# Performance work log

Hardware: AMD Instinct MI355X
Metric: run time of the kernel (lower is better)

Reference implementation:

```python
import jax, jax.numpy as jnp
from jax import lax
import numpy as np

B, H, W = 16, 512, 512
OPENING_R, EROSION_R, DILATION_R = 5, 2, 1
MIN_SIZE, AREA_THRESHOLD = 2000, 300
INF = np.int32(2 ** 30)


def _disk(r):
    # skimage.morphology.disk: x^2 + y^2 <= r^2 on a (2r+1)^2 grid
    y, x = np.mgrid[-r:r + 1, -r:r + 1]
    return jnp.asarray((x * x + y * y <= r * r).astype(np.float32))


D_OPEN, D_ERODE, D_DILATE = _disk(OPENING_R), _disk(EROSION_R), _disk(DILATION_R)


def _conv2(x, k):
    return lax.conv_general_dilated(x[None, None], k[None, None], (1, 1), 'VALID')[0, 0]


def _erode(fg, se):
    # skimage binary_erosion uses border_value=True (image border does not erode)
    r = se.shape[0] // 2
    x = jnp.pad(fg.astype(jnp.float32), r, constant_values=1.0)
    return _conv2(x, se) >= se.sum() - 0.5


def _dilate(fg, se):
    # skimage binary_dilation uses border_value=False
    r = se.shape[0] // 2
    x = jnp.pad(fg.astype(jnp.float32), r, constant_values=0.0)
    return _conv2(x, se) > 0.5


def _seg_cummin(v, reset, axis, reverse):
    # segmented cumulative-min: scan resets wherever `reset` is True (background)
    def comb(a, b):
        av, af = a
        bv, bf = b
        return jnp.where(bf, bv, jnp.minimum(av, bv)), af | bf

    vv, _ = lax.associative_scan(comb, (v, reset), axis=axis, reverse=reverse)
    return vv


def _label(fg):
    # 4-connectivity connected-component labeling via min-label propagation.
    # Each fg pixel starts with its raveled index; alternating row/col segmented
    # cummin sweeps run under while_loop until a fixed point (root id per comp).
    h, w = fg.shape
    idx = jnp.arange(h * w, dtype=jnp.int32).reshape(h, w)
    lab0 = jnp.where(fg, idx, INF)
    bg = ~fg

    def sweep(l):
        for axis in (1, 0):
            for rev in (False, True):
                l = jnp.where(fg, _seg_cummin(l, bg, axis, rev), INF)
        return l

    def body(c):
        l, _ = c
        nl = sweep(l)
        return nl, jnp.array_equal(nl, l)

    lab, _ = lax.while_loop(lambda c: ~c[1], body, (lab0, jnp.array(False)))
    seg = jnp.where(fg, lab, 0).ravel()
    sizes = jax.ops.segment_sum(fg.astype(jnp.int32).ravel(), seg, num_segments=h * w)
    ncomp = jnp.sum(sizes > 0)
    return lab, sizes, ncomp


def _remove_small_objects(fg, min_size, guard):
    lab, sizes, ncomp = _label(fg)
    px = sizes[jnp.where(fg, lab, 0)]  # component size at every fg pixel
    kept = fg & (px >= min_size)
    # original only removes small objects when label(...).max() > 1
    return jnp.where(ncomp > 1, kept, fg) if guard else kept


def _pipeline(mask):
    fg = mask > 0
    fg = _remove_small_objects(fg, MIN_SIZE, True)
    # remove_small_holes == ~remove_small_objects(~fg, area_threshold + 1)
    fg = ~_remove_small_objects(~fg, AREA_THRESHOLD + 1, False)
    fg = _erode(fg, D_ERODE)
    fg = _dilate(_erode(fg, D_OPEN), D_OPEN)  # binary_opening
    fg = _remove_small_objects(fg, MIN_SIZE, True)
    fg = _dilate(fg, D_DILATE)
    return fg.astype(jnp.float32)  # original casts to int; float32 kept for vjp parity


def setup_inputs() -> dict:
    key = jax.random.key(0)
    # blobby binary masks: threshold bilinearly-upsampled low-res noise so that
    # realistic large connected components (> min_size px) exist
    low = jax.random.uniform(key, (B, H // 16, W // 16), dtype=jnp.float32)
    blob = jax.image.resize(low, (B, H, W), method='bilinear')
    return {'inputs': (blob > 0.5).astype(jnp.float32)}


def reference(inputs):
    return jax.vmap(_pipeline)(inputs)
```

## Files before the change

kernel.cpp:

```cpp
#include <hip/hip_runtime.h>
#include <stdint.h>

#define BATCH 16
#define H 512
#define W 512
#define HW (H * W)
#define NTOT (BATCH * HW)
#define NWORDS (NTOT / 64)

#define TPB 256
#define NBLKW ((NWORDS + TPB - 1) / TPB)

#define SROWS 16
#define SWORDS 128
#define SPIX 8192
#define NSTRIPS (NWORDS / SWORDS)

__device__ __forceinline__ int find_root_c(int* L, int x) {
    int r = x, p = L[r];
    while (p != r) { r = p; p = L[r]; }
    if (L[x] != r) atomicMin(&L[x], r);
    return r;
}

__device__ void merge_uf(int* L, int a, int b) {
    while (true) {
        a = find_root_c(L, a);
        b = find_root_c(L, b);
        if (a == b) return;
        int lo = a < b ? a : b;
        int hi = a < b ? b : a;
        int old = atomicMin(&L[hi], lo);
        if (old == hi) return;
        a = lo; b = old;
    }
}

__device__ __forceinline__ int find_root_lds(int* P, int x) {
    int r = x, p = P[r];
    while (p != r) { r = p; p = P[r]; }
    return r;
}

__device__ void merge_lds(int* P, int a, int b) {
    while (true) {
        a = find_root_lds(P, a);
        b = find_root_lds(P, b);
        if (a == b) return;
        int lo = a < b ? a : b;
        int hi = a < b ? b : a;
        int old = atomicMin(&P[hi], lo);
        if (old == hi) return;
        a = lo; b = old;
    }
}

__device__ __forceinline__ int start_of(uint64_t m, int i, int cv, int base) {
    uint64_t below = i ? ((~m) & ((1ull << i) - 1)) : 0ull;
    if (below == 0) return (cv >= 0) ? cv : base;
    int hz = 63 - __builtin_clzll(below);
    return base + hz + 1;
}

__device__ uint64_t keep_word(const uint64_t* __restrict__ bits,
                              const int* __restrict__ carry, const int* __restrict__ L,
                              const int* __restrict__ sizes, const int* __restrict__ ncomp,
                              int minsz, int gw) {
    uint64_t m = bits[gw];
    uint64_t res = m;
    if (m && ncomp[gw >> 12] > 1) {
        int cv = carry[gw];
        int base = gw << 6;
        while (m) {
            int s = __builtin_ctzll(m);
            uint64_t rest = m >> s;
            uint64_t nr = ~rest;
            int len = nr ? __builtin_ctzll(nr) : (64 - s);
            uint64_t piece = ((len >= 64) ? ~0ull : ((1ull << len) - 1)) << s;
            int start = (s == 0 && cv >= 0) ? cv : (base + s);
            if (sizes[L[start]] < minsz) res &= ~piece;
            m &= ~piece;
        }
    }
    return res;
}

__device__ uint64_t fill_word(const uint64_t* __restrict__ bits,
                              const int* __restrict__ carry, const int* __restrict__ L,
                              const int* __restrict__ sizes, int minsz, int gw) {
    uint64_t fg = bits[gw];
    uint64_t bg = ~fg;
    uint64_t res = fg;
    int cv = carry[gw];
    int base = gw << 6;
    while (bg) {
        int s = __builtin_ctzll(bg);
        uint64_t rest = bg >> s;
        uint64_t nr = ~rest;
        int len = nr ? __builtin_ctzll(nr) : (64 - s);
        uint64_t piece = ((len >= 64) ? ~0ull : ((1ull << len) - 1)) << s;
        int start = (s == 0 && cv >= 0) ? cv : (base + s);
        if (sizes[L[start]] < minsz) res |= piece;
        bg &= ~piece;
    }
    return res;
}

template <int R, bool ERODE>
__device__ uint64_t morph_word_lds(const uint64_t* buf, int lrow, int w, int gyTop) {
    const uint64_t BORDER = ERODE ? ~0ull : 0ull;
    uint64_t res = ERODE ? ~0ull : 0ull;
#pragma unroll
    for (int dy = -R; dy <= R; ++dy) {
        int lr = lrow + dy;
        int gy = gyTop + lr;
        if (gy < 0 || gy >= H) continue;
        int v = R * R - dy * dy;
        int kx = 0;
        while ((kx + 1) * (kx + 1) <= v) ++kx;
        uint64_t cur = buf[lr * 8 + w];
        uint64_t prv = (w > 0) ? buf[lr * 8 + w - 1] : BORDER;
        uint64_t nxt = (w < 7) ? buf[lr * 8 + w + 1] : BORDER;
        uint64_t acc = cur;
#pragma unroll
        for (int dx = 1; dx <= kx; ++dx) {
            uint64_t right = (cur >> dx) | (nxt << (64 - dx));
            uint64_t left  = (cur << dx) | (prv >> (64 - dx));
            if (ERODE) acc &= right & left;
            else       acc |= right | left;
        }
        if (ERODE) res &= acc;
        else       res |= acc;
    }
    return res;
}

__device__ void strip_ccl_body(uint64_t m, uint64_t* sw, int* scarry, int* par,
                               int blk, int t,
                               int* __restrict__ carry, int* __restrict__ L,
                               int* __restrict__ sizes, int* __restrict__ ncomp) {
    sw[t] = m;
    __syncthreads();

    if (t < SROWS) {
        int cv = -1;
        for (int i = 0; i < 8; ++i) {
            int lw = t * 8 + i;
            scarry[lw] = cv;
            uint64_t w = sw[lw];
            if (w >> 63) {
                uint64_t z = ~w;
                if (z == 0) { if (cv < 0) cv = lw << 6; }
                else { int hz = 63 - __builtin_clzll(z); cv = (lw << 6) + hz + 1; }
            } else cv = -1;
        }
    }
    __syncthreads();

    int cv = scarry[t];
    carry[blk * SWORDS + t] = (cv >= 0) ? (blk * SPIX + cv) : -1;
    int lbase = t << 6;
    uint64_t starts = m & ~((m << 1) | ((cv >= 0) ? 1ull : 0ull));
    uint64_t ss = starts;
    while (ss) {
        int s = __builtin_ctzll(ss);
        par[lbase + s] = lbase + s;
        ss &= ss - 1;
    }
    __syncthreads();

    if (t >= 8 && m) {
        uint64_t up = sw[t - 8];
        uint64_t cand = m & up;
        if (cand) {
            uint64_t curprev = (t & 7) ? sw[t - 1] : 0ull;
            uint64_t upprev  = (t & 7) ? sw[t - 9] : 0ull;
            uint64_t curl = (m << 1) | (curprev >> 63);
            uint64_t upl  = (up << 1) | (upprev >> 63);
            cand &= ~(curl & upl);
            int cvu = scarry[t - 8];
            while (cand) {
                int i = __builtin_ctzll(cand);
                int sP = start_of(m, i, cv, lbase);
                int sQ = start_of(up, i, cvu, lbase - 512);
                merge_lds(par, sP, sQ);
                cand &= cand - 1;
            }
        }
    }
    __syncthreads();

    int gpix = blk * SPIX;
    ss = starts;
    while (ss) {
        int s = __builtin_ctzll(ss);
        int ls = lbase + s;
        int r = find_root_lds(par, ls);
        L[gpix + ls] = gpix + r;
        if (r == ls) sizes[gpix + ls] = 0;
        ss &= ss - 1;
    }
    if (t == 0 && (blk & 31) == 0) ncomp[blk >> 5] = 0;
}


__global__ void k_thresh_pack4(const float4* __restrict__ in4,
                               uint64_t* __restrict__ bits) {
    int q = blockIdx.x * blockDim.x + threadIdx.x;
    if (q >= NTOT / 4) return;
    float4 v = in4[q];
    uint32_t nib = (v.x > 0.0f ? 1u : 0u) | (v.y > 0.0f ? 2u : 0u) |
                   (v.z > 0.0f ? 4u : 0u) | (v.w > 0.0f ? 8u : 0u);
    uint64_t val = (uint64_t)nib << (4 * (threadIdx.x & 15));
    val |= __shfl_xor(val, 1);
    val |= __shfl_xor(val, 2);
    val |= __shfl_xor(val, 4);
    val |= __shfl_xor(val, 8);
    if ((threadIdx.x & 15) == 0) bits[q >> 4] = val;
}

__global__ void k_strip_ccl(const uint64_t* __restrict__ bits, int inv,
                            int* __restrict__ carry, int* __restrict__ L,
                            int* __restrict__ sizes, int* __restrict__ ncomp) {
    __shared__ uint64_t sw[SWORDS];
    __shared__ int scarry[SWORDS];
    __shared__ int par[SPIX];
    int blk = blockIdx.x;
    int t = threadIdx.x;
    uint64_t inv64 = inv ? ~0ull : 0ull;
    uint64_t m = bits[blk * SWORDS + t] ^ inv64;
    strip_ccl_body(m, sw, scarry, par, blk, t, carry, L, sizes, ncomp);
}

__global__ void k_keep_strip(const uint64_t* __restrict__ bits,
                             const int* __restrict__ carryIn, const int* __restrict__ Lin,
                             const int* __restrict__ sizesIn, const int* __restrict__ ncompIn,
                             uint64_t* __restrict__ outBits,
                             int* __restrict__ carryOut, int* __restrict__ Lout,
                             int* __restrict__ sizesOut, int* __restrict__ ncompOut) {
    __shared__ uint64_t sw[SWORDS];
    __shared__ int scarry[SWORDS];
    __shared__ int par[SPIX];
    int blk = blockIdx.x;
    int t = threadIdx.x;
    int gw = blk * SWORDS + t;
    uint64_t kw = keep_word(bits, carryIn, Lin, sizesIn, ncompIn, 2000, gw);
    outBits[gw] = kw;
    strip_ccl_body(~kw, sw, scarry, par, blk, t, carryOut, Lout, sizesOut, ncompOut);
}

__global__ void k_merge_bound(const uint64_t* __restrict__ bits, int inv,
                              const int* __restrict__ carry, int* __restrict__ L) {
    int tid = threadIdx.x;
    if (tid >= 248) return;
    int img = blockIdx.x;
    int y = ((tid >> 3) + 1) * SROWS;
    int w = tid & 7;
    int gw = img * 4096 + y * 8 + w;
    uint64_t inv64 = inv ? ~0ull : 0ull;
    uint64_t cur = bits[gw] ^ inv64;
    uint64_t up  = bits[gw - 8] ^ inv64;
    uint64_t cand = cur & up;
    if (!cand) return;
    uint64_t curprev = w ? (bits[gw - 1] ^ inv64) : 0ull;
    uint64_t upprev  = w ? (bits[gw - 9] ^ inv64) : 0ull;
    uint64_t curl = (cur << 1) | (curprev >> 63);
    uint64_t upl  = (up << 1)  | (upprev >> 63);
    cand &= ~(curl & upl);
    if (!cand) return;
    int cvc = carry[gw], cvu = carry[gw - 8];
    int base = gw << 6;
    while (cand) {
        int i = __builtin_ctzll(cand);
        int sP = start_of(cur, i, cvc, base);
        int sQ = start_of(up, i, cvu, base - W);
        merge_uf(L, sP, sQ);
        cand &= cand - 1;
    }
}

__global__ void k_flatten_count(const uint64_t* __restrict__ bits, int inv,
                                const int* __restrict__ carry, int* __restrict__ L,
                                int* __restrict__ sizes, int* __restrict__ ncomp) {
    __shared__ int hk[128];
    __shared__ int hv[128];
    for (int i = threadIdx.x; i < 128; i += TPB) { hk[i] = -1; hv[i] = 0; }
    __syncthreads();

    int gw = blockIdx.x * blockDim.x + threadIdx.x;
    if (gw < NWORDS) {
        uint64_t inv64 = inv ? ~0ull : 0ull;
        uint64_t m = bits[gw] ^ inv64;
        if (m) {
            int cv = carry[gw];
            int base = gw << 6;
            while (m) {
                int s = __builtin_ctzll(m);
                uint64_t rest = m >> s;
                uint64_t nr = ~rest;
                int len = nr ? __builtin_ctzll(nr) : (64 - s);
                uint64_t piece = ((len >= 64) ? ~0ull : ((1ull << len) - 1)) << s;
                bool initial = !(s == 0 && cv >= 0);
                int start = initial ? (base + s) : cv;
                int r = find_root_c(L, start);
                if (initial && r == start) atomicAdd(&ncomp[gw >> 12], 1);
                int cnt = __popcll(piece);
                uint32_t h = ((uint32_t)r * 2654435761u) >> 25;
                bool done = false;
                for (int tt = 0; tt < 16; ++tt) {
                    int slot = (h + tt) & 127;
                    int k = hk[slot];
                    if (k == -1) k = atomicCAS(&hk[slot], -1, r);
                    if (k == -1 || k == r) { atomicAdd(&hv[slot], cnt); done = true; break; }
                }
                if (!done) atomicAdd(&sizes[r], cnt);
                m &= ~piece;
            }
        }
    }
    __syncthreads();
    for (int i = threadIdx.x; i < 128; i += TPB)
        if (hk[i] != -1) atomicAdd(&sizes[hk[i]], hv[i]);
}

__global__ void k_fill_morph_ccl(const uint64_t* __restrict__ bits,
                                 const int* __restrict__ carryB, const int* __restrict__ LB,
                                 const int* __restrict__ sizesB,
                                 uint64_t* __restrict__ bits3,
                                 int* __restrict__ carryA, int* __restrict__ LA,
                                 int* __restrict__ sizesA, int* __restrict__ ncompA) {
    __shared__ uint64_t sw[SWORDS];
    __shared__ int scarry[SWORDS];
    __shared__ union {
        int par[SPIX];
        struct { uint64_t A[320]; uint64_t B[320]; } mo;
    } U;
    int s = blockIdx.x;
    int t = threadIdx.x;
    int img = s >> 5, si = s & 31;
    int gyTop = si * 16 - 12;

    for (int lw = t; lw < 320; lw += SWORDS) {
        int gy = gyTop + (lw >> 3);
        int w = lw & 7;
        uint64_t v = 0;
        if (gy >= 0 && gy < H)
            v = fill_word(bits, carryB, LB, sizesB, 301, img * 4096 + gy * 8 + w);
        U.mo.A[lw] = v;
    }
    __syncthreads();
    for (int lw = t; lw < 320; lw += SWORDS) {
        int lr = lw >> 3;
        if (lr >= 2 && lr <= 37) U.mo.B[lw] = morph_word_lds<2, true>(U.mo.A, lr, lw & 7, gyTop);
    }
    __syncthreads();
    for (int lw = t; lw < 320; lw += SWORDS) {
        int lr = lw >> 3;
        if (lr >= 7 && lr <= 32) U.mo.A[lw] = morph_word_lds<5, true>(U.mo.B, lr, lw & 7, gyTop);
    }
    __syncthreads();
    for (int lw = t; lw < 320; lw += SWORDS) {
        int lr = lw >> 3;
        if (lr >= 12 && lr <= 27) U.mo.B[lw] = morph_word_lds<5, false>(U.mo.A, lr, lw & 7, gyTop);
    }
    __syncthreads();
    uint64_t m3 = U.mo.B[t + 96];
    bits3[s * SWORDS + t] = m3;
    strip_ccl_body(m3, sw, scarry, U.par, s, t, carryA, LA, sizesA, ncompA);
}

__global__ void k_keep_dilate_float(const uint64_t* __restrict__ bits,
                                    const int* __restrict__ carry, const int* __restrict__ L,
                                    const int* __restrict__ sizes, const int* __restrict__ ncomp,
                                    float* __restrict__ out) {
    __shared__ uint64_t kb[10 * 8];
    __shared__ uint64_t db[8 * 8];
    int blk = blockIdx.x;
    int img = blk >> 6;
    int s = blk & 63;
    int y0 = s * 8;
    int t = threadIdx.x;

    if (t < 80) {
        int lr = t >> 3;
        int w = t & 7;
        int gy = y0 - 1 + lr;
        uint64_t v = 0;
        if (gy >= 0 && gy < H)
            v = keep_word(bits, carry, L, sizes, ncomp, 2000, img * 4096 + gy * 8 + w);
        kb[t] = v;
    }
    __syncthreads();
    if (t < 64) {
        int r = t >> 3, w = t & 7;
        uint64_t cur = kb[(r + 1) * 8 + w];
        uint64_t up  = kb[r * 8 + w];
        uint64_t dn  = kb[(r + 2) * 8 + w];
        uint64_t prv = w ? kb[(r + 1) * 8 + w - 1] : 0ull;
        uint64_t nxt = (w < 7) ? kb[(r + 1) * 8 + w + 1] : 0ull;
        db[t] = cur | up | dn | (cur << 1) | (prv >> 63) | (cur >> 1) | (nxt << 63);
    }
    __syncthreads();

    int q0 = t * 16;
    uint64_t wd = db[q0 >> 6];
    int sh = q0 & 63;
    float4* o = (float4*)(out + (size_t)img * HW + (size_t)y0 * W + q0);
#pragma unroll
    for (int k = 0; k < 4; ++k) {
        uint32_t nib = (uint32_t)(wd >> (sh + k * 4)) & 0xFu;
        float4 f;
        f.x = (nib & 1u) ? 1.0f : 0.0f;
        f.y = (nib & 2u) ? 1.0f : 0.0f;
        f.z = (nib & 4u) ? 1.0f : 0.0f;
        f.w = (nib & 8u) ? 1.0f : 0.0f;
        o[k] = f;
    }
}

extern "C" void kernel_launch(void* const* d_in, const int* in_sizes, int n_in,
                              void* d_out, int out_size, void* d_ws, size_t ws_size,
                              hipStream_t stream) {
    const float* in = (const float*)d_in[0];
    float* out = (float*)d_out;

    uint8_t* ws = (uint8_t*)d_ws;
    int* LA      = (int*)ws;
    int* sizesA  = (int*)(ws + (size_t)NTOT * 4);
    int* LB      = (int*)(ws + (size_t)NTOT * 8);
    int* sizesB  = (int*)(ws + (size_t)NTOT * 12);
    uint64_t* bits1 = (uint64_t*)(ws + (size_t)NTOT * 16);
    uint64_t* bits2 = bits1 + NWORDS;
    uint64_t* bits3 = bits2 + NWORDS;
    int* carryA = (int*)(bits3 + NWORDS);
    int* carryB = carryA + NWORDS;
    int* ncompA = carryB + NWORDS;
    int* ncompB = ncompA + BATCH;

    k_thresh_pack4<<<(NTOT / 4 + TPB - 1) / TPB, TPB, 0, stream>>>((const float4*)in, bits1);

    k_strip_ccl<<<NSTRIPS, SWORDS, 0, stream>>>(bits1, 0, carryA, LA, sizesA, ncompA);
    k_merge_bound<<<BATCH, 256, 0, stream>>>(bits1, 0, carryA, LA);
    k_flatten_count<<<NBLKW, TPB, 0, stream>>>(bits1, 0, carryA, LA, sizesA, ncompA);

    k_keep_strip<<<NSTRIPS, SWORDS, 0, stream>>>(bits1, carryA, LA, sizesA, ncompA,
                                                 bits2, carryB, LB, sizesB, ncompB);
    k_merge_bound<<<BATCH, 256, 0, stream>>>(bits2, 1, carryB, LB);
    k_flatten_count<<<NBLKW, TPB, 0, stream>>>(bits2, 1, carryB, LB, sizesB, ncompB);

    k_fill_morph_ccl<<<NSTRIPS, SWORDS, 0, stream>>>(bits2, carryB, LB, sizesB,
                                                     bits3, carryA, LA, sizesA, ncompA);
    k_merge_bound<<<BATCH, 256, 0, stream>>>(bits3, 0, carryA, LA);
    k_flatten_count<<<NBLKW, TPB, 0, stream>>>(bits3, 0, carryA, LA, sizesA, ncompA);

    k_keep_dilate_float<<<BATCH * 64, TPB, 0, stream>>>(bits3, carryA, LA, sizesA, ncompA, out);
}
```

Baseline: 201.3 us.

## Fuse whole pipeline into one persistent per-image kernel with run-based labels

Replaces the chain of about eleven kernel launches with a single kernel using one 1024-thread workgroup per image, running every stage back to back separated by workgroup barriers. Union-find labels are now indexed by run id rather than pixel, built with a prefix-scan over run counts, and merged with workgroup-scope atomics in global memory. The morphology stages read whole images from global memory instead of haloed LDS strips. This removes launch overhead and inter-kernel round trips, but uses only 16 workgroups on a many-CU GPU, so most of the device sits idle and the serial work per image grows.

```diff
diff --git a/kernel.cpp b/kernel.cpp
--- a/kernel.cpp
+++ b/kernel.cpp
@@ -7,120 +7,109 @@
 #define HW (H * W)
 #define NTOT (BATCH * HW)
 #define NWORDS (NTOT / 64)
-
-#define TPB 256
-#define NBLKW ((NWORDS + TPB - 1) / TPB)
-
+#define IMGW 4096
+#define IMGQ 65536
 #define SROWS 16
 #define SWORDS 128
-#define SPIX 8192
-#define NSTRIPS (NWORDS / SWORDS)
-
-__device__ __forceinline__ int find_root_c(int* L, int x) {
-    int r = x, p = L[r];
-    while (p != r) { r = p; p = L[r]; }
-    if (L[x] != r) atomicMin(&L[x], r);
+#define MAXR 4096
+#define NR (BATCH * 32 * MAXR)
+#define WALK_LIMIT (1 << 16)
+
+static __device__ __forceinline__ int aldw(const int* p) {
+    return __hip_atomic_load((int*)p, __ATOMIC_RELAXED, __HIP_MEMORY_SCOPE_WORKGROUP);
+}
+static __device__ __forceinline__ int aminw(int* p, int v) {
+    return __hip_atomic_fetch_min(p, v, __ATOMIC_RELAXED, __HIP_MEMORY_SCOPE_WORKGROUP);
+}
+static __device__ __forceinline__ int aaddw(int* p, int v) {
+    return __hip_atomic_fetch_add(p, v, __ATOMIC_RELAXED, __HIP_MEMORY_SCOPE_WORKGROUP);
+}
+
+static __device__ __forceinline__ int find_root(int* L, int x) {
+    int r = x, p = aldw(&L[r]), g = 0;
+    while (p != r && ++g < WALK_LIMIT) { r = p; p = aldw(&L[r]); }
+    if (aldw(&L[x]) != r) aminw(&L[x], r);
     return r;
 }
 
-__device__ void merge_uf(int* L, int a, int b) {
-    while (true) {
-        a = find_root_c(L, a);
-        b = find_root_c(L, b);
+static __device__ void merge_uf(int* L, int a, int b) {
+    int g = 0;
+    while (++g < WALK_LIMIT) {
+        a = find_root(L, a);
+        b = find_root(L, b);
         if (a == b) return;
         int lo = a < b ? a : b;
         int hi = a < b ? b : a;
-        int old = atomicMin(&L[hi], lo);
+        int old = aminw(&L[hi], lo);
         if (old == hi) return;
         a = lo; b = old;
     }
 }
 
-__device__ __forceinline__ int find_root_lds(int* P, int x) {
-    int r = x, p = P[r];
-    while (p != r) { r = p; p = P[r]; }
-    return r;
-}
-
-__device__ void merge_lds(int* P, int a, int b) {
-    while (true) {
-        a = find_root_lds(P, a);
-        b = find_root_lds(P, b);
-        if (a == b) return;
-        int lo = a < b ? a : b;
-        int hi = a < b ? b : a;
-        int old = atomicMin(&P[hi], lo);
-        if (old == hi) return;
-        a = lo; b = old;
-    }
-}
-
-__device__ __forceinline__ int start_of(uint64_t m, int i, int cv, int base) {
+static __device__ __forceinline__ int run_of(uint64_t m, int i, int cvrid, int wr) {
     uint64_t below = i ? ((~m) & ((1ull << i) - 1)) : 0ull;
-    if (below == 0) return (cv >= 0) ? cv : base;
-    int hz = 63 - __builtin_clzll(below);
-    return base + hz + 1;
-}
-
-__device__ uint64_t keep_word(const uint64_t* __restrict__ bits,
-                              const int* __restrict__ carry, const int* __restrict__ L,
-                              const int* __restrict__ sizes, const int* __restrict__ ncomp,
-                              int minsz, int gw) {
-    uint64_t m = bits[gw];
-    uint64_t res = m;
-    if (m && ncomp[gw >> 12] > 1) {
-        int cv = carry[gw];
-        int base = gw << 6;
-        while (m) {
-            int s = __builtin_ctzll(m);
-            uint64_t rest = m >> s;
-            uint64_t nr = ~rest;
-            int len = nr ? __builtin_ctzll(nr) : (64 - s);
-            uint64_t piece = ((len >= 64) ? ~0ull : ((1ull << len) - 1)) << s;
-            int start = (s == 0 && cv >= 0) ? cv : (base + s);
-            if (sizes[L[start]] < minsz) res &= ~piece;
-            m &= ~piece;
-        }
-    }
-    return res;
-}
-
-__device__ uint64_t fill_word(const uint64_t* __restrict__ bits,
-                              const int* __restrict__ carry, const int* __restrict__ L,
-                              const int* __restrict__ sizes, int minsz, int gw) {
-    uint64_t fg = bits[gw];
-    uint64_t bg = ~fg;
-    uint64_t res = fg;
-    int cv = carry[gw];
-    int base = gw << 6;
-    while (bg) {
-        int s = __builtin_ctzll(bg);
-        uint64_t rest = bg >> s;
+    if (below == 0) return (cvrid >= 0) ? cvrid : wr;
+    int s = 64 - __builtin_clzll(below);
+    uint64_t starts = m & ~((m << 1) | ((cvrid >= 0) ? 1ull : 0ull));
+    return wr + __popcll(starts & ((1ull << s) - 1));
+}
+
+static __device__ __forceinline__ int run_of_l(uint64_t m, int i, int cv,
+                                               uint64_t starts, int wb) {
+    uint64_t below = i ? ((~m) & ((1ull << i) - 1)) : 0ull;
+    if (below == 0) return (cv >= 0) ? cv : wb;
+    int s = 64 - __builtin_clzll(below);
+    return wb + __popcll(starts & ((1ull << s) - 1));
+}
+
+static __device__ uint64_t keep_word_g(uint64_t m, int cvg, int wrg,
+                                       const int* L, const int* S, int minsz) {
+    uint64_t res = m, rem = m; int rk = 0;
+    while (rem) {
+        int s = __builtin_ctzll(rem);
+        uint64_t rest = rem >> s;
         uint64_t nr = ~rest;
         int len = nr ? __builtin_ctzll(nr) : (64 - s);
         uint64_t piece = ((len >= 64) ? ~0ull : ((1ull << len) - 1)) << s;
-        int start = (s == 0 && cv >= 0) ? cv : (base + s);
-        if (sizes[L[start]] < minsz) res |= piece;
-        bg &= ~piece;
+        bool ini = !(s == 0 && cvg >= 0);
+        int rid = ini ? (wrg + rk) : cvg; rk += ini ? 1 : 0;
+        if (aldw(&S[aldw(&L[rid])]) < minsz) res &= ~piece;
+        rem &= ~piece;
     }
     return res;
 }
 
+static __device__ uint64_t fill_word_g(uint64_t fg, int cvg, int wrg,
+                                       const int* L, const int* S, int minsz) {
+    uint64_t res = fg, rem = ~fg; int rk = 0;
+    while (rem) {
+        int s = __builtin_ctzll(rem);
+        uint64_t rest = rem >> s;
+        uint64_t nr = ~rest;
+        int len = nr ? __builtin_ctzll(nr) : (64 - s);
+        uint64_t piece = ((len >= 64) ? ~0ull : ((1ull << len) - 1)) << s;
+        bool ini = !(s == 0 && cvg >= 0);
+        int rid = ini ? (wrg + rk) : cvg; rk += ini ? 1 : 0;
+        if (aldw(&S[aldw(&L[rid])]) < minsz) res |= piece;
+        rem &= ~piece;
+    }
+    return res;
+}
+
 template <int R, bool ERODE>
-__device__ uint64_t morph_word_lds(const uint64_t* buf, int lrow, int w, int gyTop) {
+static __device__ uint64_t morph_word_g(const uint64_t* ib, int row, int w) {
     const uint64_t BORDER = ERODE ? ~0ull : 0ull;
     uint64_t res = ERODE ? ~0ull : 0ull;
 #pragma unroll
     for (int dy = -R; dy <= R; ++dy) {
-        int lr = lrow + dy;
-        int gy = gyTop + lr;
+        int gy = row + dy;
         if (gy < 0 || gy >= H) continue;
         int v = R * R - dy * dy;
         int kx = 0;
         while ((kx + 1) * (kx + 1) <= v) ++kx;
-        uint64_t cur = buf[lr * 8 + w];
-        uint64_t prv = (w > 0) ? buf[lr * 8 + w - 1] : BORDER;
-        uint64_t nxt = (w < 7) ? buf[lr * 8 + w + 1] : BORDER;
+        uint64_t cur = ib[gy * 8 + w];
+        uint64_t prv = (w > 0) ? ib[gy * 8 + w - 1] : BORDER;
+        uint64_t nxt = (w < 7) ? ib[gy * 8 + w + 1] : BORDER;
         uint64_t acc = cur;
 #pragma unroll
         for (int dx = 1; dx <= kx; ++dx) {
@@ -135,286 +124,268 @@
     return res;
 }
 
-__device__ void strip_ccl_body(uint64_t m, uint64_t* sw, int* scarry, int* par,
-                               int blk, int t,
-                               int* __restrict__ carry, int* __restrict__ L,
-                               int* __restrict__ sizes, int* __restrict__ ncomp) {
-    sw[t] = m;
-    __syncthreads();
-
-    if (t < SROWS) {
-        int cv = -1;
-        for (int i = 0; i < 8; ++i) {
-            int lw = t * 8 + i;
-            scarry[lw] = cv;
-            uint64_t w = sw[lw];
-            if (w >> 63) {
-                uint64_t z = ~w;
-                if (z == 0) { if (cv < 0) cv = lw << 6; }
-                else { int hz = 63 - __builtin_clzll(z); cv = (lw << 6) + hz + 1; }
-            } else cv = -1;
-        }
-    }
-    __syncthreads();
-
-    int cv = scarry[t];
-    carry[blk * SWORDS + t] = (cv >= 0) ? (blk * SPIX + cv) : -1;
-    int lbase = t << 6;
-    uint64_t starts = m & ~((m << 1) | ((cv >= 0) ? 1ull : 0ull));
-    uint64_t ss = starts;
-    while (ss) {
-        int s = __builtin_ctzll(ss);
-        par[lbase + s] = lbase + s;
-        ss &= ss - 1;
-    }
-    __syncthreads();
-
-    if (t >= 8 && m) {
-        uint64_t up = sw[t - 8];
-        uint64_t cand = m & up;
+static __device__ void ccl_image(int img, int t, const uint64_t* bits, uint64_t inv64,
+                                 int* carry, int* wordrun, int* L, int* S, int* ncomp,
+                                 uint64_t (*ssw)[SWORDS], int (*sscar)[SWORDS],
+                                 int (*scnt)[SWORDS], int (*swb)[SWORDS], int* wsum) {
+    int sg = t >> 7, tt = t & 127;
+    int lane = t & 63;
+    if (t == 0) ncomp[img] = 0;
+
+    for (int sr = 0; sr < 4; ++sr) {
+        int si = sr * 8 + sg;
+        int sid = img * 32 + si;
+        int gb = sid * MAXR;
+        int gw = sid * SWORDS + tt;
+        uint64_t m = bits[gw] ^ inv64;
+        ssw[sg][tt] = m;
+        __syncthreads();
+
+        bool cont = (tt & 7) ? ((ssw[sg][tt - 1] >> 63) != 0) : false;
+        int c = __popcll(m & ~(m << 1));
+        if ((m & 1ull) && cont) --c;
+
+        int x = c;
+#pragma unroll
+        for (int off = 1; off < 64; off <<= 1) {
+            int y = __shfl_up(x, off);
+            if (lane >= off) x += y;
+        }
+        if (tt == 63) wsum[sg] = x;
+        __syncthreads();
+        if (tt >= 64) x += wsum[sg];
+        swb[sg][tt] = x;
+        scnt[sg][tt] = c;
+        __syncthreads();
+
+        if (tt < SROWS) {
+            int cv = -1;
+            for (int i = 0; i < 8; ++i) {
+                int lw = tt * 8 + i;
+                sscar[sg][lw] = cv;
+                uint64_t w = ssw[sg][lw];
+                if (w >> 63) { if (scnt[sg][lw] > 0) cv = swb[sg][lw] - 1; }
+                else cv = -1;
+            }
+        }
+        __syncthreads();
+
+        int cv = sscar[sg][tt];
+        int wb = swb[sg][tt] - scnt[sg][tt];
+        carry[gw] = (cv >= 0) ? (gb + cv) : -1;
+        wordrun[gw] = gb + wb;
+        int nruns = swb[sg][127];
+        for (int i = tt; i < nruns; i += 128) { L[gb + i] = gb + i; S[gb + i] = 0; }
+        __syncthreads();
+
+        if (tt >= 8 && m) {
+            uint64_t up = ssw[sg][tt - 8];
+            uint64_t cand = m & up;
+            if (cand) {
+                uint64_t curprev = (tt & 7) ? ssw[sg][tt - 1] : 0ull;
+                uint64_t upprev  = (tt & 7) ? ssw[sg][tt - 9] : 0ull;
+                uint64_t curl = (m << 1) | (curprev >> 63);
+                uint64_t upl  = (up << 1) | (upprev >> 63);
+                cand &= ~(curl & upl);
+                int cvu = sscar[sg][tt - 8];
+                int wbu = swb[sg][tt - 8] - scnt[sg][tt - 8];
+                uint64_t starts  = m & ~((m << 1) | ((cv >= 0) ? 1ull : 0ull));
+                uint64_t startsU = up & ~((up << 1) | ((cvu >= 0) ? 1ull : 0ull));
+                while (cand) {
+                    int i = __builtin_ctzll(cand);
+                    int sP = gb + run_of_l(m, i, cv, starts, wb);
+                    int sQ = gb + run_of_l(up, i, cvu, startsU, wbu);
+                    merge_uf(L, sP, sQ);
+                    cand &= cand - 1;
+                }
+            }
+        }
+        __syncthreads();
+    }
+
+    if (t < 992) {
+        int item = t >> 2, j = t & 3;
+        int b = item >> 3, w = item & 7;
+        int gw = img * IMGW + (b + 1) * 128 + w;
+        uint64_t cur = bits[gw] ^ inv64;
+        uint64_t up  = bits[gw - 8] ^ inv64;
+        uint64_t cand = cur & up;
         if (cand) {
-            uint64_t curprev = (t & 7) ? sw[t - 1] : 0ull;
-            uint64_t upprev  = (t & 7) ? sw[t - 9] : 0ull;
-            uint64_t curl = (m << 1) | (curprev >> 63);
+            uint64_t curprev = w ? (bits[gw - 1] ^ inv64) : 0ull;
+            uint64_t upprev  = w ? (bits[gw - 9] ^ inv64) : 0ull;
+            uint64_t curl = (cur << 1) | (curprev >> 63);
             uint64_t upl  = (up << 1) | (upprev >> 63);
             cand &= ~(curl & upl);
-            int cvu = scarry[t - 8];
-            while (cand) {
-                int i = __builtin_ctzll(cand);
-                int sP = start_of(m, i, cv, lbase);
-                int sQ = start_of(up, i, cvu, lbase - 512);
-                merge_lds(par, sP, sQ);
-                cand &= cand - 1;
+            if (cand) {
+                int cvc = carry[gw], wrc = wordrun[gw];
+                int cvu = carry[gw - 8], wru = wordrun[gw - 8];
+                int idx = 0;
+                while (cand) {
+                    int i = __builtin_ctzll(cand);
+                    if ((idx & 3) == j) {
+                        int sP = run_of(cur, i, cvc, wrc);
+                        int sQ = run_of(up, i, cvu, wru);
+                        merge_uf(L, sP, sQ);
+                    }
+                    ++idx;
+                    cand &= cand - 1;
+                }
             }
         }
     }
     __syncthreads();
 
-    int gpix = blk * SPIX;
-    ss = starts;
-    while (ss) {
-        int s = __builtin_ctzll(ss);
-        int ls = lbase + s;
-        int r = find_root_lds(par, ls);
-        L[gpix + ls] = gpix + r;
-        if (r == ls) sizes[gpix + ls] = 0;
-        ss &= ss - 1;
-    }
-    if (t == 0 && (blk & 31) == 0) ncomp[blk >> 5] = 0;
-}
-
-
-__global__ void k_thresh_pack4(const float4* __restrict__ in4,
-                               uint64_t* __restrict__ bits) {
-    int q = blockIdx.x * blockDim.x + threadIdx.x;
-    if (q >= NTOT / 4) return;
-    float4 v = in4[q];
-    uint32_t nib = (v.x > 0.0f ? 1u : 0u) | (v.y > 0.0f ? 2u : 0u) |
-                   (v.z > 0.0f ? 4u : 0u) | (v.w > 0.0f ? 8u : 0u);
-    uint64_t val = (uint64_t)nib << (4 * (threadIdx.x & 15));
-    val |= __shfl_xor(val, 1);
-    val |= __shfl_xor(val, 2);
-    val |= __shfl_xor(val, 4);
-    val |= __shfl_xor(val, 8);
-    if ((threadIdx.x & 15) == 0) bits[q >> 4] = val;
-}
-
-__global__ void k_strip_ccl(const uint64_t* __restrict__ bits, int inv,
-                            int* __restrict__ carry, int* __restrict__ L,
-                            int* __restrict__ sizes, int* __restrict__ ncomp) {
-    __shared__ uint64_t sw[SWORDS];
-    __shared__ int scarry[SWORDS];
-    __shared__ int par[SPIX];
-    int blk = blockIdx.x;
+    for (int k = 0; k < 4; ++k) {
+        int lw = t * 4 + k;
+        int gw = img * IMGW + lw;
+        uint64_t m = bits[gw] ^ inv64;
+        if (!m) continue;
+        int cvg = carry[gw], wrg = wordrun[gw];
+        int rk = 0;
+        uint64_t rem = m;
+        while (rem) {
+            int s = __builtin_ctzll(rem);
+            uint64_t rest = rem >> s;
+            uint64_t nr = ~rest;
+            int len = nr ? __builtin_ctzll(nr) : (64 - s);
+            uint64_t piece = ((len >= 64) ? ~0ull : ((1ull << len) - 1)) << s;
+            bool ini = !(s == 0 && cvg >= 0);
+            int rid = ini ? (wrg + rk) : cvg; rk += ini ? 1 : 0;
+            int r = find_root(L, rid);
+            if (ini && r == rid) aaddw(&ncomp[img], 1);
+            aaddw(&S[r], __popcll(piece));
+            rem &= ~piece;
+        }
+    }
+    __syncthreads();
+}
+
+__global__ __launch_bounds__(1024, 1) void k_img(
+        const float4* __restrict__ in4, float* __restrict__ out,
+        int* LA, int* SA, int* LB, int* SB,
+        uint64_t* bits1, uint64_t* bits2, uint64_t* bits3,
+        int* carryA, int* carryB, int* wrA, int* wrB,
+        int* ncompA, int* ncompB) {
+    __shared__ uint64_t ssw[8][SWORDS];
+    __shared__ int sscar[8][SWORDS];
+    __shared__ int scnt[8][SWORDS];
+    __shared__ int swb[8][SWORDS];
+    __shared__ int wsum[8];
+    __shared__ int shnc;
+    int img = blockIdx.x;
     int t = threadIdx.x;
-    uint64_t inv64 = inv ? ~0ull : 0ull;
-    uint64_t m = bits[blk * SWORDS + t] ^ inv64;
-    strip_ccl_body(m, sw, scarry, par, blk, t, carry, L, sizes, ncomp);
-}
-
-__global__ void k_keep_strip(const uint64_t* __restrict__ bits,
-                             const int* __restrict__ carryIn, const int* __restrict__ Lin,
-                             const int* __restrict__ sizesIn, const int* __restrict__ ncompIn,
-                             uint64_t* __restrict__ outBits,
-                             int* __restrict__ carryOut, int* __restrict__ Lout,
-                             int* __restrict__ sizesOut, int* __restrict__ ncompOut) {
-    __shared__ uint64_t sw[SWORDS];
-    __shared__ int scarry[SWORDS];
-    __shared__ int par[SPIX];
-    int blk = blockIdx.x;
-    int t = threadIdx.x;
-    int gw = blk * SWORDS + t;
-    uint64_t kw = keep_word(bits, carryIn, Lin, sizesIn, ncompIn, 2000, gw);
-    outBits[gw] = kw;
-    strip_ccl_body(~kw, sw, scarry, par, blk, t, carryOut, Lout, sizesOut, ncompOut);
-}
-
-__global__ void k_merge_bound(const uint64_t* __restrict__ bits, int inv,
-                              const int* __restrict__ carry, int* __restrict__ L) {
-    int tid = threadIdx.x;
-    if (tid >= 248) return;
-    int img = blockIdx.x;
-    int y = ((tid >> 3) + 1) * SROWS;
-    int w = tid & 7;
-    int gw = img * 4096 + y * 8 + w;
-    uint64_t inv64 = inv ? ~0ull : 0ull;
-    uint64_t cur = bits[gw] ^ inv64;
-    uint64_t up  = bits[gw - 8] ^ inv64;
-    uint64_t cand = cur & up;
-    if (!cand) return;
-    uint64_t curprev = w ? (bits[gw - 1] ^ inv64) : 0ull;
-    uint64_t upprev  = w ? (bits[gw - 9] ^ inv64) : 0ull;
-    uint64_t curl = (cur << 1) | (curprev >> 63);
-    uint64_t upl  = (up << 1)  | (upprev >> 63);
-    cand &= ~(curl & upl);
-    if (!cand) return;
-    int cvc = carry[gw], cvu = carry[gw - 8];
-    int base = gw << 6;
-    while (cand) {
-        int i = __builtin_ctzll(cand);
-        int sP = start_of(cur, i, cvc, base);
-        int sQ = start_of(up, i, cvu, base - W);
-        merge_uf(L, sP, sQ);
-        cand &= cand - 1;
-    }
-}
-
-__global__ void k_flatten_count(const uint64_t* __restrict__ bits, int inv,
-                                const int* __restrict__ carry, int* __restrict__ L,
-                                int* __restrict__ sizes, int* __restrict__ ncomp) {
-    __shared__ int hk[128];
-    __shared__ int hv[128];
-    for (int i = threadIdx.x; i < 128; i += TPB) { hk[i] = -1; hv[i] = 0; }
-    __syncthreads();
-
-    int gw = blockIdx.x * blockDim.x + threadIdx.x;
-    if (gw < NWORDS) {
-        uint64_t inv64 = inv ? ~0ull : 0ull;
-        uint64_t m = bits[gw] ^ inv64;
-        if (m) {
-            int cv = carry[gw];
-            int base = gw << 6;
-            while (m) {
-                int s = __builtin_ctzll(m);
-                uint64_t rest = m >> s;
-                uint64_t nr = ~rest;
-                int len = nr ? __builtin_ctzll(nr) : (64 - s);
-                uint64_t piece = ((len >= 64) ? ~0ull : ((1ull << len) - 1)) << s;
-                bool initial = !(s == 0 && cv >= 0);
-                int start = initial ? (base + s) : cv;
-                int r = find_root_c(L, start);
-                if (initial && r == start) atomicAdd(&ncomp[gw >> 12], 1);
-                int cnt = __popcll(piece);
-                uint32_t h = ((uint32_t)r * 2654435761u) >> 25;
-                bool done = false;
-                for (int tt = 0; tt < 16; ++tt) {
-                    int slot = (h + tt) & 127;
-                    int k = hk[slot];
-                    if (k == -1) k = atomicCAS(&hk[slot], -1, r);
-                    if (k == -1 || k == r) { atomicAdd(&hv[slot], cnt); done = true; break; }
-                }
-                if (!done) atomicAdd(&sizes[r], cnt);
-                m &= ~piece;
-            }
-        }
-    }
-    __syncthreads();
-    for (int i = threadIdx.x; i < 128; i += TPB)
-        if (hk[i] != -1) atomicAdd(&sizes[hk[i]], hv[i]);
-}
-
-__global__ void k_fill_morph_ccl(const uint64_t* __restrict__ bits,
-                                 const int* __restrict__ carryB, const int* __restrict__ LB,
-                                 const int* __restrict__ sizesB,
-                                 uint64_t* __restrict__ bits3,
-                                 int* __restrict__ carryA, int* __restrict__ LA,
-                                 int* __restrict__ sizesA, int* __restrict__ ncompA) {
-    __shared__ uint64_t sw[SWORDS];
-    __shared__ int scarry[SWORDS];
-    __shared__ union {
-        int par[SPIX];
-        struct { uint64_t A[320]; uint64_t B[320]; } mo;
-    } U;
-    int s = blockIdx.x;
-    int t = threadIdx.x;
-    int img = s >> 5, si = s & 31;
-    int gyTop = si * 16 - 12;
-
-    for (int lw = t; lw < 320; lw += SWORDS) {
-        int gy = gyTop + (lw >> 3);
-        int w = lw & 7;
-        uint64_t v = 0;
-        if (gy >= 0 && gy < H)
-            v = fill_word(bits, carryB, LB, sizesB, 301, img * 4096 + gy * 8 + w);
-        U.mo.A[lw] = v;
-    }
-    __syncthreads();
-    for (int lw = t; lw < 320; lw += SWORDS) {
-        int lr = lw >> 3;
-        if (lr >= 2 && lr <= 37) U.mo.B[lw] = morph_word_lds<2, true>(U.mo.A, lr, lw & 7, gyTop);
-    }
-    __syncthreads();
-    for (int lw = t; lw < 320; lw += SWORDS) {
-        int lr = lw >> 3;
-        if (lr >= 7 && lr <= 32) U.mo.A[lw] = morph_word_lds<5, true>(U.mo.B, lr, lw & 7, gyTop);
-    }
-    __syncthreads();
-    for (int lw = t; lw < 320; lw += SWORDS) {
-        int lr = lw >> 3;
-        if (lr >= 12 && lr <= 27) U.mo.B[lw] = morph_word_lds<5, false>(U.mo.A, lr, lw & 7, gyTop);
-    }
-    __syncthreads();
-    uint64_t m3 = U.mo.B[t + 96];
-    bits3[s * SWORDS + t] = m3;
-    strip_ccl_body(m3, sw, scarry, U.par, s, t, carryA, LA, sizesA, ncompA);
-}
-
-__global__ void k_keep_dilate_float(const uint64_t* __restrict__ bits,
-                                    const int* __restrict__ carry, const int* __restrict__ L,
-                                    const int* __restrict__ sizes, const int* __restrict__ ncomp,
-                                    float* __restrict__ out) {
-    __shared__ uint64_t kb[10 * 8];
-    __shared__ uint64_t db[8 * 8];
-    int blk = blockIdx.x;
-    int img = blk >> 6;
-    int s = blk & 63;
-    int y0 = s * 8;
-    int t = threadIdx.x;
-
-    if (t < 80) {
-        int lr = t >> 3;
-        int w = t & 7;
-        int gy = y0 - 1 + lr;
-        uint64_t v = 0;
-        if (gy >= 0 && gy < H)
-            v = keep_word(bits, carry, L, sizes, ncomp, 2000, img * 4096 + gy * 8 + w);
-        kb[t] = v;
-    }
-    __syncthreads();
-    if (t < 64) {
-        int r = t >> 3, w = t & 7;
-        uint64_t cur = kb[(r + 1) * 8 + w];
-        uint64_t up  = kb[r * 8 + w];
-        uint64_t dn  = kb[(r + 2) * 8 + w];
-        uint64_t prv = w ? kb[(r + 1) * 8 + w - 1] : 0ull;
-        uint64_t nxt = (w < 7) ? kb[(r + 1) * 8 + w + 1] : 0ull;
-        db[t] = cur | up | dn | (cur << 1) | (prv >> 63) | (cur >> 1) | (nxt << 63);
-    }
-    __syncthreads();
-
-    int q0 = t * 16;
-    uint64_t wd = db[q0 >> 6];
-    int sh = q0 & 63;
-    float4* o = (float4*)(out + (size_t)img * HW + (size_t)y0 * W + q0);
-#pragma unroll
+
+    for (int it = 0; it < 64; ++it) {
+        int q = it * 1024 + t;
+        float4 v = in4[img * IMGQ + q];
+        uint32_t nib = (v.x > 0.0f ? 1u : 0u) | (v.y > 0.0f ? 2u : 0u) |
+                       (v.z > 0.0f ? 4u : 0u) | (v.w > 0.0f ? 8u : 0u);
+        uint64_t val = (uint64_t)nib << (4 * (t & 15));
+        val |= __shfl_xor(val, 1);
+        val |= __shfl_xor(val, 2);
+        val |= __shfl_xor(val, 4);
+        val |= __shfl_xor(val, 8);
+        if ((t & 15) == 0) bits1[img * IMGW + (q >> 4)] = val;
+    }
+    __syncthreads();
+
+    ccl_image(img, t, bits1, 0ull, carryA, wrA, LA, SA, ncompA,
+              ssw, sscar, scnt, swb, wsum);
+
+    if (t == 0) shnc = aldw(&ncompA[img]);
+    __syncthreads();
+    {
+        int nc = shnc;
+        for (int k = 0; k < 4; ++k) {
+            int gw = img * IMGW + t * 4 + k;
+            uint64_t m = bits1[gw];
+            uint64_t kw = m;
+            if (m && nc > 1)
+                kw = keep_word_g(m, carryA[gw], wrA[gw], LA, SA, 2000);
+            bits2[gw] = kw;
+        }
+    }
+    __syncthreads();
+
+    ccl_image(img, t, bits2, ~0ull, carryB, wrB, LB, SB, ncompB,
+              ssw, sscar, scnt, swb, wsum);
+
     for (int k = 0; k < 4; ++k) {
-        uint32_t nib = (uint32_t)(wd >> (sh + k * 4)) & 0xFu;
+        int gw = img * IMGW + t * 4 + k;
+        bits1[gw] = fill_word_g(bits2[gw], carryB[gw], wrB[gw], LB, SB, 301);
+    }
+    __syncthreads();
+
+    {
+        const uint64_t* ib = bits1 + img * IMGW;
+        uint64_t* ob = bits2 + img * IMGW;
+        for (int k = 0; k < 4; ++k) {
+            int lw = t * 4 + k;
+            ob[lw] = morph_word_g<2, true>(ib, lw >> 3, lw & 7);
+        }
+    }
+    __syncthreads();
+    {
+        const uint64_t* ib = bits2 + img * IMGW;
+        uint64_t* ob = bits1 + img * IMGW;
+        for (int k = 0; k < 4; ++k) {
+            int lw = t * 4 + k;
+            ob[lw] = morph_word_g<5, true>(ib, lw >> 3, lw & 7);
+        }
+    }
+    __syncthreads();
+    {
+        const uint64_t* ib = bits1 + img * IMGW;
+        uint64_t* ob = bits3 + img * IMGW;
+        for (int k = 0; k < 4; ++k) {
+            int lw = t * 4 + k;
+            ob[lw] = morph_word_g<5, false>(ib, lw >> 3, lw & 7);
+        }
+    }
+    __syncthreads();
+
+    ccl_image(img, t, bits3, 0ull, carryA, wrA, LA, SA, ncompA,
+              ssw, sscar, scnt, swb, wsum);
+
+    if (t == 0) shnc = aldw(&ncompA[img]);
+    __syncthreads();
+    {
+        int nc = shnc;
+        for (int k = 0; k < 4; ++k) {
+            int gw = img * IMGW + t * 4 + k;
+            uint64_t m = bits3[gw];
+            uint64_t kw = m;
+            if (m && nc > 1)
+                kw = keep_word_g(m, carryA[gw], wrA[gw], LA, SA, 2000);
+            bits1[gw] = kw;
+        }
+    }
+    __syncthreads();
+
+    for (int k = 0; k < 4; ++k) {
+        int lw = t * 4 + k;
+        int row = lw >> 3, w = lw & 7;
+        int gw = img * IMGW + lw;
+        uint64_t cur = bits1[gw];
+        uint64_t up  = row ? bits1[gw - 8] : 0ull;
+        uint64_t dn  = (row < H - 1) ? bits1[gw + 8] : 0ull;
+        uint64_t prv = w ? bits1[gw - 1] : 0ull;
+        uint64_t nxt = (w < 7) ? bits1[gw + 1] : 0ull;
+        bits2[gw] = cur | up | dn | (cur << 1) | (prv >> 63) |
+                    (cur >> 1) | (nxt << 63);
+    }
+    __syncthreads();
+
+    for (int it = 0; it < 64; ++it) {
+        int q = it * 1024 + t;
+        uint64_t d = bits2[img * IMGW + (q >> 4)];
+        uint32_t nib = (uint32_t)(d >> ((q & 15) * 4)) & 0xFu;
         float4 f;
         f.x = (nib & 1u) ? 1.0f : 0.0f;
         f.y = (nib & 2u) ? 1.0f : 0.0f;
         f.z = (nib & 4u) ? 1.0f : 0.0f;
         f.w = (nib & 8u) ? 1.0f : 0.0f;
-        o[k] = f;
+        ((float4*)out)[img * IMGQ + q] = f;
     }
 }
 
@@ -426,32 +397,22 @@
 
     uint8_t* ws = (uint8_t*)d_ws;
     int* LA      = (int*)ws;
-    int* sizesA  = (int*)(ws + (size_t)NTOT * 4);
-    int* LB      = (int*)(ws + (size_t)NTOT * 8);
-    int* sizesB  = (int*)(ws + (size_t)NTOT * 12);
-    uint64_t* bits1 = (uint64_t*)(ws + (size_t)NTOT * 16);
+    int* SA      = LA + NR;
+    int* LB      = SA + NR;
+    int* SB      = LB + NR;
+    uint64_t* bits1 = (uint64_t*)(SB + NR);
     uint64_t* bits2 = bits1 + NWORDS;
     uint64_t* bits3 = bits2 + NWORDS;
-    int* carryA = (int*)(bits3 + NWORDS);
-    int* carryB = carryA + NWORDS;
-    int* ncompA = carryB + NWORDS;
-    int* ncompB = ncompA + BATCH;
-
-    k_thresh_pack4<<<(NTOT / 4 + TPB - 1) / TPB, TPB, 0, stream>>>((const float4*)in, bits1);
-
-    k_strip_ccl<<<NSTRIPS, SWORDS, 0, stream>>>(bits1, 0, carryA, LA, sizesA, ncompA);
-    k_merge_bound<<<BATCH, 256, 0, stream>>>(bits1, 0, carryA, LA);
-    k_flatten_count<<<NBLKW, TPB, 0, stream>>>(bits1, 0, carryA, LA, sizesA, ncompA);
-
-    k_keep_strip<<<NSTRIPS, SWORDS, 0, stream>>>(bits1, carryA, LA, sizesA, ncompA,
-                                                 bits2, carryB, LB, sizesB, ncompB);
-    k_merge_bound<<<BATCH, 256, 0, stream>>>(bits2, 1, carryB, LB);
-    k_flatten_count<<<NBLKW, TPB, 0, stream>>>(bits2, 1, carryB, LB, sizesB, ncompB);
-
-    k_fill_morph_ccl<<<NSTRIPS, SWORDS, 0, stream>>>(bits2, carryB, LB, sizesB,
-                                                     bits3, carryA, LA, sizesA, ncompA);
-    k_merge_bound<<<BATCH, 256, 0, stream>>>(bits3, 0, carryA, LA);
-    k_flatten_count<<<NBLKW, TPB, 0, stream>>>(bits3, 0, carryA, LA, sizesA, ncompA);
-
-    k_keep_dilate_float<<<BATCH * 64, TPB, 0, stream>>>(bits3, carryA, LA, sizesA, ncompA, out);
-}
+    int* carryA  = (int*)(bits3 + NWORDS);
+    int* carryB  = carryA + NWORDS;
+    int* wrA     = carryB + NWORDS;
+    int* wrB     = wrA + NWORDS;
+    int* ncompA  = wrB + NWORDS;
+    int* ncompB  = ncompA + BATCH;
+
+    k_img<<<BATCH, 1024, 0, stream>>>((const float4*)in, out,
+                                      LA, SA, LB, SB,
+                                      bits1, bits2, bits3,
+                                      carryA, carryB, wrA, wrB,
+                                      ncompA, ncompB);
+}
```

After: 687.6 us. 3.42x slower.
